# Kernel tuning notes

Hardware: AMD Instinct MI355X
Metric: run time of the kernel (lower is better)

## Reference

```python
import jax, jax.numpy as jnp
import numpy as np

N_HEAD = 16
HIDDEN = 1024

def setup_inputs() -> dict:
    key = jax.random.key(0)
    ks = jax.random.split(key, 4)
    B, T, D = 2, 2048, HIDDEN
    x = jax.random.normal(ks[0], (B, T, D), dtype=jnp.float32)
    attention_mask = jnp.zeros((B, 1, 1, T), dtype=jnp.float32)  # additive mask
    w_attn = jax.random.normal(ks[1], (D, 3 * D), dtype=jnp.float32) * (1.0 / np.sqrt(D))
    b_attn = jnp.zeros((3 * D,), dtype=jnp.float32)
    w_proj = jax.random.normal(ks[2], (D, D), dtype=jnp.float32) * (1.0 / np.sqrt(D))
    b_proj = jnp.zeros((D,), dtype=jnp.float32)
    return {"x": x, "attention_mask": attention_mask,
            "w_attn": w_attn, "b_attn": b_attn,
            "w_proj": w_proj, "b_proj": b_proj}

def reference(x, attention_mask, w_attn, b_attn, w_proj, b_proj):
    B, T, D = x.shape
    H = N_HEAD
    hd = D // H
    qkv = x @ w_attn + b_attn                      # [B,T,3D]
    q, k, v = jnp.split(qkv, 3, axis=-1)
    q = q.reshape(B, T, H, hd)
    k = k.reshape(B, T, H, hd)
    v = v.reshape(B, T, H, hd)
    qk = jnp.einsum('BFNH,BTNH->BNFT', q, k) / jnp.sqrt(jnp.asarray(hd, qk_dtype := q.dtype))
    # NOTE: source adds the mask twice (once unconditionally, once inside the None-check)
    attn_weights = qk + attention_mask + attention_mask
    attn_probs = jax.nn.softmax(attn_weights, axis=-1)  # dropout(0.01) is identity at inference
    attn_out = jnp.einsum('BNFT,BTNH->BFNH', attn_probs, v)
    attn_out = attn_out.reshape(B, T, D)
    return attn_out @ w_proj + b_proj
```

## Files before the change

### kernel.cpp

```cpp
#include <hip/hip_runtime.h>
#include <hip/hip_bf16.h>

#define T_SEQ 2048
#define D_MODEL 1024
#define N_HEADS 16

typedef _Float16 half8 __attribute__((ext_vector_type(8)));
typedef _Float16 half4 __attribute__((ext_vector_type(4)));
typedef _Float16 half2v __attribute__((ext_vector_type(2)));
typedef float floatx4 __attribute__((ext_vector_type(4)));
typedef unsigned short ushort4v __attribute__((ext_vector_type(4)));
typedef unsigned short ushort8v __attribute__((ext_vector_type(8)));

#define LOG2E 1.44269504088896f

__device__ __forceinline__ unsigned short f32_to_bf16(float f) {
  unsigned u = __builtin_bit_cast(unsigned, f);
  u = u + 0x7FFFu + ((u >> 16) & 1u);
  return (unsigned short)(u >> 16);
}
__device__ __forceinline__ float bf16_to_f32(unsigned short h) {
  unsigned u = ((unsigned)h) << 16;
  return __builtin_bit_cast(float, u);
}
__device__ __forceinline__ half2v pk_f16(float a, float b) {
  return __builtin_bit_cast(half2v, __builtin_amdgcn_cvt_pkrtz(a, b));
}

__device__ __forceinline__ void load16_lds(const _Float16* g, _Float16* lds_base, int lane) {
#if __has_builtin(__builtin_amdgcn_global_load_lds)
  __builtin_amdgcn_global_load_lds(
      (const __attribute__((address_space(1))) void*)g,
      (__attribute__((address_space(3))) void*)lds_base, 16, 0, 0);
#else
  *(half8*)(lds_base + lane * 8) = *(const half8*)g;
#endif
}

__global__ void k_detect(const unsigned short* __restrict__ x, int* __restrict__ flag) {
  __shared__ int cnt;
  if (threadIdx.x == 0) cnt = 0;
  __syncthreads();
  unsigned short v = x[(size_t)threadIdx.x * 2];
  int e = (v >> 7) & 0xFF;
  int ok = (v == 0) || (e >= 100 && e <= 150);
  atomicAdd(&cnt, ok);
  __syncthreads();
  if (threadIdx.x == 0) *flag = (cnt >= 192) ? 1 : 0;
}

__global__ void k_cvt_h8(const void* __restrict__ in, _Float16* __restrict__ out,
                         int n8, const int* __restrict__ flag) {
  int f = *flag;
  int i = blockIdx.x * 256 + threadIdx.x;
  if (i >= n8) return;
  half8 o;
  if (f) {
    ushort8v u = ((const ushort8v*)in)[i];
#pragma unroll
    for (int e = 0; e < 8; ++e) o[e] = (_Float16)bf16_to_f32(u[e]);
  } else {
    floatx4 a = ((const floatx4*)in)[2 * i];
    floatx4 b = ((const floatx4*)in)[2 * i + 1];
#pragma unroll
    for (int e = 0; e < 4; ++e) { o[e] = (_Float16)a[e]; o[e + 4] = (_Float16)b[e]; }
  }
  ((half8*)out)[i] = o;
}

__global__ void k_cvt3(const void* __restrict__ ba, const void* __restrict__ bp,
                       const void* __restrict__ mk, float* __restrict__ baF,
                       float* __restrict__ bpF, float* __restrict__ mask2,
                       const int* __restrict__ flag) {
  int f = *flag;
  int i = blockIdx.x * 256 + threadIdx.x;
  auto cv = [&](const void* p, int j) {
    return f ? bf16_to_f32(((const unsigned short*)p)[j]) : ((const float*)p)[j];
  };
  if (i < 3072) baF[i] = cv(ba, i);
  else if (i < 4096) bpF[i - 3072] = cv(bp, i - 3072);
  else mask2[i - 4096] = cv(mk, i - 4096) * (2.0f * LOG2E);
}

__global__ __launch_bounds__(256) void k_transpose2(
    const void* __restrict__ inA, _Float16* __restrict__ outA,
    const void* __restrict__ inB, _Float16* __restrict__ outB,
    const int* __restrict__ flag) {
  __shared__ float tile[32][33];
  int f = *flag;
  const void* in;
  _Float16* out;
  int N, bid;
  if (blockIdx.x < 3072) { in = inA; out = outA; N = 3072; bid = blockIdx.x; }
  else { in = inB; out = outB; N = 1024; bid = blockIdx.x - 3072; }
  const int K = 1024;
  int nb = N >> 5;
  int bx = bid % nb, by = bid / nb;
  int n0 = bx << 5, k0 = by << 5;
  int c = threadIdx.x & 31, r = threadIdx.x >> 5;
  const float* fin = (const float*)in;
  const unsigned short* uin = (const unsigned short*)in;
#pragma unroll
  for (int i = 0; i < 4; ++i) {
    int kk = r + i * 8;
    size_t idx = (size_t)(k0 + kk) * N + n0 + c;
    tile[kk][c] = f ? bf16_to_f32(uin[idx]) : fin[idx];
  }
  __syncthreads();
#pragma unroll
  for (int i = 0; i < 4; ++i) {
    int nn = r + i * 8;
    out[(size_t)(n0 + nn) * K + k0 + c] = (_Float16)tile[c][nn];
  }
}

template <int TM>
__global__ __launch_bounds__(256) void k_gemm(
    const _Float16* __restrict__ A, const _Float16* __restrict__ BT,
    const float* __restrict__ bias, void* __restrict__ D0,
    void* __restrict__ D1, void* __restrict__ D2,
    int M, int N, int K, int outKind, const int* __restrict__ flag) {
  constexpr int IM = TM / 32;
  __shared__ _Float16 As[TM * 32] __attribute__((aligned(16)));
  __shared__ _Float16 Bs[128 * 32] __attribute__((aligned(16)));
  const int tid = threadIdx.x;
  const int wave = tid >> 6, lane = tid & 63;
  const int ln = lane & 15, quad = lane >> 4;
  const int bm = blockIdx.y * TM, bn = blockIdx.x * 128;
  const int wm = (wave & 1) * (TM / 2), wn = (wave >> 1) * 64;

  const int r0 = tid >> 2, k0 = (tid & 3) * 8;
  const int r1 = (tid + 256) >> 2, k1 = (tid & 3) * 8;
  _Float16* As0 = As + (size_t)(wave * 64) * 8;
  _Float16* As1 = As + (size_t)(wave * 64 + 256) * 8;
  _Float16* Bs0 = Bs + (size_t)(wave * 64) * 8;
  _Float16* Bs1 = Bs + (size_t)(wave * 64 + 256) * 8;
  const _Float16* Ag0 = A + (size_t)(bm + r0) * K + k0;
  const _Float16* Ag1 = A + (size_t)(bm + r1) * K + k1;
  const _Float16* Bg0 = BT + (size_t)(bn + r0) * K + k0;
  const _Float16* Bg1 = BT + (size_t)(bn + r1) * K + k1;

  floatx4 acc[IM][4] = {};

  for (int kt = 0; kt < K; kt += 32) {
    __syncthreads();
    load16_lds(Ag0 + kt, As0, lane);
    if constexpr (TM == 128) load16_lds(Ag1 + kt, As1, lane);
    load16_lds(Bg0 + kt, Bs0, lane);
    load16_lds(Bg1 + kt, Bs1, lane);
    __syncthreads();
    half8 af[IM], bf[4];
#pragma unroll
    for (int i = 0; i < IM; ++i)
      af[i] = *(const half8*)(As + (wm + i * 16 + ln) * 32 + quad * 8);
#pragma unroll
    for (int j = 0; j < 4; ++j)
      bf[j] = *(const half8*)(Bs + (wn + j * 16 + ln) * 32 + quad * 8);
#pragma unroll
    for (int i = 0; i < IM; ++i)
#pragma unroll
      for (int j = 0; j < 4; ++j)
        acc[i][j] = __builtin_amdgcn_mfma_f32_16x16x32_f16(af[i], bf[j], acc[i][j], 0, 0, 0);
  }

  if (outKind == 0) {
    _Float16* Qs = (_Float16*)D0;
    _Float16* Ks = (_Float16*)D1;
    _Float16* Vt = (_Float16*)D2;
    const float qsc = 0.125f * LOG2E;
#pragma unroll
    for (int i = 0; i < IM; ++i) {
      int rbase = bm + wm + i * 16 + quad * 4;
      int sect = rbase >> 10;
      int cfeat = rbase & 1023;
      int h = cfeat >> 6, hd = cfeat & 63;
      float bv[4];
#pragma unroll
      for (int r = 0; r < 4; ++r) bv[r] = bias[rbase + r];
#pragma unroll
      for (int j = 0; j < 4; ++j) {
        int col = bn + wn + j * 16 + ln;
        int b = col >> 11, t = col & 2047;
        size_t bh = (size_t)b * N_HEADS + h;
        float v[4];
#pragma unroll
        for (int r = 0; r < 4; ++r) v[r] = acc[i][j][r] + bv[r];
        if (sect == 0) {
          half4 q;
#pragma unroll
          for (int r = 0; r < 4; ++r) q[r] = (_Float16)(v[r] * qsc);
          *(half4*)(Qs + (bh * T_SEQ + t) * 64 + hd) = q;
        } else if (sect == 1) {
          half4 kk4;
#pragma unroll
          for (int r = 0; r < 4; ++r) kk4[r] = (_Float16)v[r];
          *(half4*)(Ks + (bh * T_SEQ + t) * 64 + hd) = kk4;
        } else {
#pragma unroll
          for (int r = 0; r < 4; ++r)
            Vt[(bh * 64 + hd + r) * T_SEQ + t] = (_Float16)v[r];
        }
      }
    }
  } else {
    int mode = (*flag) ? 2 : 1;
#pragma unroll
    for (int i = 0; i < IM; ++i) {
      int rbase = bm + wm + i * 16 + quad * 4;
      float bv[4];
#pragma unroll
      for (int r = 0; r < 4; ++r) bv[r] = bias[rbase + r];
#pragma unroll
      for (int j = 0; j < 4; ++j) {
        int col = bn + wn + j * 16 + ln;
        float v[4];
#pragma unroll
        for (int r = 0; r < 4; ++r) v[r] = acc[i][j][r] + bv[r];
        if (mode == 1) {
          floatx4 o = {v[0], v[1], v[2], v[3]};
          *(floatx4*)((float*)D0 + (size_t)col * M + rbase) = o;
        } else {
          ushort4v o;
#pragma unroll
          for (int r = 0; r < 4; ++r) o[r] = f32_to_bf16(v[r]);
          *(ushort4v*)((unsigned short*)D0 + (size_t)col * M + rbase) = o;
        }
      }
    }
  }
}

__global__ __launch_bounds__(256) void k_flash(
    const _Float16* __restrict__ Qs, const _Float16* __restrict__ Ks,
    const _Float16* __restrict__ Vt, const float* __restrict__ mask2,
    _Float16* __restrict__ O) {
  __shared__ _Float16 Kl[2][64 * 64] __attribute__((aligned(16)));
  __shared__ _Float16 Vl[2][64 * 64] __attribute__((aligned(16)));
  __shared__ _Float16 Pl[4][16 * 64] __attribute__((aligned(16)));
  const int tid = threadIdx.x, wave = tid >> 6, lane = tid & 63;
  const int ln = lane & 15, quad = lane >> 4;
  const int id = blockIdx.x;
  const int qc = id & 31, h = (id >> 5) & 15, b = id >> 9;
  const size_t bh = (size_t)b * N_HEADS + h;
  const _Float16* Qb = Qs + bh * T_SEQ * 64;
  const _Float16* Kb = Ks + bh * T_SEQ * 64;
  const _Float16* Vb = Vt + bh * 64 * T_SEQ;
  const int q0 = qc * 64 + wave * 16;

  half8 qf[2];
#pragma unroll
  for (int kk = 0; kk < 2; ++kk)
    qf[kk] = *(const half8*)(Qb + (size_t)(q0 + ln) * 64 + kk * 32 + quad * 8);

  floatx4 Oacc[4] = {};
  float m0 = 0.f, l_i = 0.f;

  const int sr = tid >> 3, scn = (tid & 7) ^ (sr & 7);
  const _Float16* kp0 = Kb + (size_t)sr * 64 + scn * 8;
  const _Float16* kp1 = kp0 + 32 * 64;
  const _Float16* vp0 = Vb + (size_t)sr * T_SEQ + scn * 8;
  const _Float16* vp1 = vp0 + 32 * T_SEQ;
  const float* mq = mask2 + (size_t)b * T_SEQ + quad * 4;

  const int ksw0 = ((quad) ^ (ln & 7)) * 8;
  const int ksw1 = ((4 + quad) ^ (ln & 7)) * 8;
  _Float16* Pw = &Pl[wave][0];
  const int lnx = ln & 7;

  {
    _Float16* K0 = &Kl[0][0] + (size_t)wave * 512;
    _Float16* V0 = &Vl[0][0] + (size_t)wave * 512;
    load16_lds(kp0, K0, lane);
    load16_lds(kp1, K0 + 2048, lane);
    load16_lds(vp0, V0, lane);
    load16_lds(vp1, V0 + 2048, lane);
    kp0 += 64 * 64; kp1 += 64 * 64; vp0 += 64; vp1 += 64;
  }

  for (int t = 0; t < 32; ++t) {
    const int cur = t & 1;
    __syncthreads();
    if (t + 1 < 32) {
      _Float16* K0 = &Kl[cur ^ 1][0] + (size_t)wave * 512;
      _Float16* V0 = &Vl[cur ^ 1][0] + (size_t)wave * 512;
      load16_lds(kp0, K0, lane);
      load16_lds(kp1, K0 + 2048, lane);
      load16_lds(vp0, V0, lane);
      load16_lds(vp1, V0 + 2048, lane);
      kp0 += 64 * 64; kp1 += 64 * 64; vp0 += 64; vp1 += 64;
    }
    const _Float16* Kc = &Kl[cur][0];
    const _Float16* Vc = &Vl[cur][0];

    floatx4 s[4];
#pragma unroll
    for (int j = 0; j < 4; ++j) {
      floatx4 z = *(const floatx4*)(mq + j * 16);
      half8 kf0 = *(const half8*)(Kc + (j * 16 + ln) * 64 + ksw0);
      z = __builtin_amdgcn_mfma_f32_16x16x32_f16(kf0, qf[0], z, 0, 0, 0);
      half8 kf1 = *(const half8*)(Kc + (j * 16 + ln) * 64 + ksw1);
      z = __builtin_amdgcn_mfma_f32_16x16x32_f16(kf1, qf[1], z, 0, 0, 0);
      s[j] = z;
    }
    mq += 64;

    if (t == 0) {
      float tmax = -__builtin_inff();
#pragma unroll
      for (int j = 0; j < 4; ++j)
#pragma unroll
        for (int r = 0; r < 4; ++r) tmax = fmaxf(tmax, s[j][r]);
      tmax = fmaxf(tmax, __shfl_xor(tmax, 16, 64));
      tmax = fmaxf(tmax, __shfl_xor(tmax, 32, 64));
      m0 = fmaxf(tmax, -50.f);
    }

#pragma unroll
    for (int j = 0; j < 4; ++j)
#pragma unroll
      for (int r = 0; r < 4; ++r) {
        float p = __builtin_amdgcn_exp2f(s[j][r] - m0);
        s[j][r] = p;
        l_i += p;
      }

#pragma unroll
    for (int j = 0; j < 4; ++j) {
      half2v p01 = pk_f16(s[j][0], s[j][1]);
      half2v p23 = pk_f16(s[j][2], s[j][3]);
      half4 pk = {p01[0], p01[1], p23[0], p23[1]};
      int c = j * 2 + (quad >> 1);
      *(half4*)(Pw + ln * 64 + (c ^ lnx) * 8 + (quad & 1) * 4) = pk;
    }
    asm volatile("" ::: "memory");
#pragma unroll
    for (int kk = 0; kk < 2; ++kk) {
      half8 pf = *(const half8*)(Pw + ln * 64 + ((kk * 4 + quad) ^ lnx) * 8);
      int ks = kk ? ksw1 : ksw0;
#pragma unroll
      for (int jd = 0; jd < 4; ++jd) {
        half8 vf = *(const half8*)(Vc + (jd * 16 + ln) * 64 + ks);
        Oacc[jd] = __builtin_amdgcn_mfma_f32_16x16x32_f16(vf, pf, Oacc[jd], 0, 0, 0);
      }
    }
  }

  l_i += __shfl_xor(l_i, 16, 64);
  l_i += __shfl_xor(l_i, 32, 64);
  float inv = 1.f / l_i;
#pragma unroll
  for (int jd = 0; jd < 4; ++jd) {
    half4 ov;
#pragma unroll
    for (int r = 0; r < 4; ++r) ov[r] = (_Float16)(Oacc[jd][r] * inv);
    *(half4*)(O + ((size_t)b * T_SEQ + q0 + ln) * D_MODEL + h * 64 + jd * 16 + quad * 4) = ov;
  }
}

extern "C" void kernel_launch(void* const* d_in, const int* in_sizes, int n_in,
                              void* d_out, int out_size, void* d_ws, size_t ws_size,
                              hipStream_t stream) {
  const void* x      = d_in[0];
  const void* amask  = d_in[1];
  const void* w_attn = d_in[2];
  const void* b_attn = d_in[3];
  const void* w_proj = d_in[4];
  const void* b_proj = d_in[5];

  char* ws = (char*)d_ws;
  size_t off = 0;
  auto alloc = [&](size_t bytes) {
    void* p = ws + off;
    off += (bytes + 255) & ~(size_t)255;
    return p;
  };
  int* flag        = (int*)alloc(256);
  _Float16* Xh     = (_Float16*)alloc((size_t)4096 * 1024 * 2);
  _Float16* WaT    = (_Float16*)alloc((size_t)3072 * 1024 * 2);
  _Float16* WpT    = (_Float16*)alloc((size_t)1024 * 1024 * 2);
  float* baF       = (float*)alloc(3072 * 4);
  float* bpF       = (float*)alloc(1024 * 4);
  float* mask2     = (float*)alloc(4096 * 4);
  _Float16* Qs     = (_Float16*)alloc((size_t)4096 * 1024 * 2);
  _Float16* Ks     = (_Float16*)alloc((size_t)4096 * 1024 * 2);
  _Float16* Vt     = (_Float16*)alloc((size_t)4096 * 1024 * 2);
  _Float16* AttnH  = (_Float16*)alloc((size_t)4096 * 1024 * 2);

  k_detect<<<1, 256, 0, stream>>>((const unsigned short*)x, flag);
  k_cvt_h8<<<(4096 * 1024 / 8) / 256, 256, 0, stream>>>(x, Xh, 4096 * 1024 / 8, flag);
  k_transpose2<<<3072 + 1024, 256, 0, stream>>>(w_attn, WaT, w_proj, WpT, flag);
  k_cvt3<<<32, 256, 0, stream>>>(b_attn, b_proj, amask, baF, bpF, mask2, flag);

  dim3 g1(4096 / 128, 3072 / 128);
  k_gemm<128><<<g1, 256, 0, stream>>>(WaT, Xh, baF, Qs, Ks, Vt, 3072, 4096, 1024, 0, flag);

  k_flash<<<1024, 256, 0, stream>>>(Qs, Ks, Vt, mask2, AttnH);

  dim3 g2(4096 / 128, 1024 / 128);
  k_gemm<128><<<g2, 256, 0, stream>>>(WpT, AttnH, bpF, d_out, nullptr, nullptr, 1024, 4096, 1024, 1, flag);
}
```

Baseline: 223.1 us.

## Switch flash attention to 32x32x16 MFMA with register-shuffled P operand

The attention kernel moves from 16x16x32 to 32x32x16 MFMA tiles. Each wave now handles 32 query rows, so a block covers 128 queries and the grid halves to 512 blocks. The softmax probabilities no longer round-trip through LDS; they are packed to f16 and swapped across wave halves with cross-lane shuffles to form the B operand directly. This halves K/V LDS reloads per query, removes the P staging buffer, and cuts LDS traffic. In exchange it uses more accumulator registers and gives fewer blocks to spread across the CUs.

```diff
diff --git a/kernel.cpp b/kernel.cpp
--- a/kernel.cpp
+++ b/kernel.cpp
@@ -9,8 +9,10 @@
 typedef _Float16 half4 __attribute__((ext_vector_type(4)));
 typedef _Float16 half2v __attribute__((ext_vector_type(2)));
 typedef float floatx4 __attribute__((ext_vector_type(4)));
+typedef float floatx16 __attribute__((ext_vector_type(16)));
 typedef unsigned short ushort4v __attribute__((ext_vector_type(4)));
 typedef unsigned short ushort8v __attribute__((ext_vector_type(8)));
+typedef unsigned int uintx4 __attribute__((ext_vector_type(4)));
 
 #define LOG2E 1.44269504088896f
 
@@ -236,23 +238,22 @@
     _Float16* __restrict__ O) {
   __shared__ _Float16 Kl[2][64 * 64] __attribute__((aligned(16)));
   __shared__ _Float16 Vl[2][64 * 64] __attribute__((aligned(16)));
-  __shared__ _Float16 Pl[4][16 * 64] __attribute__((aligned(16)));
   const int tid = threadIdx.x, wave = tid >> 6, lane = tid & 63;
-  const int ln = lane & 15, quad = lane >> 4;
+  const int l31 = lane & 31, h5 = lane >> 5, swz = l31 & 7;
   const int id = blockIdx.x;
-  const int qc = id & 31, h = (id >> 5) & 15, b = id >> 9;
-  const size_t bh = (size_t)b * N_HEADS + h;
+  const int qc = id & 15, hh = (id >> 4) & 15, b = id >> 8;
+  const size_t bh = (size_t)b * N_HEADS + hh;
   const _Float16* Qb = Qs + bh * T_SEQ * 64;
   const _Float16* Kb = Ks + bh * T_SEQ * 64;
   const _Float16* Vb = Vt + bh * 64 * T_SEQ;
-  const int q0 = qc * 64 + wave * 16;
-
-  half8 qf[2];
-#pragma unroll
-  for (int kk = 0; kk < 2; ++kk)
-    qf[kk] = *(const half8*)(Qb + (size_t)(q0 + ln) * 64 + kk * 32 + quad * 8);
-
-  floatx4 Oacc[4] = {};
+  const int q0 = qc * 128 + wave * 32;
+
+  half8 qf[4];
+#pragma unroll
+  for (int ks = 0; ks < 4; ++ks)
+    qf[ks] = *(const half8*)(Qb + (size_t)(q0 + l31) * 64 + ks * 16 + h5 * 8);
+
+  floatx16 Oacc[2] = {};
   float m0 = 0.f, l_i = 0.f;
 
   const int sr = tid >> 3, scn = (tid & 7) ^ (sr & 7);
@@ -260,12 +261,7 @@
   const _Float16* kp1 = kp0 + 32 * 64;
   const _Float16* vp0 = Vb + (size_t)sr * T_SEQ + scn * 8;
   const _Float16* vp1 = vp0 + 32 * T_SEQ;
-  const float* mq = mask2 + (size_t)b * T_SEQ + quad * 4;
-
-  const int ksw0 = ((quad) ^ (ln & 7)) * 8;
-  const int ksw1 = ((4 + quad) ^ (ln & 7)) * 8;
-  _Float16* Pw = &Pl[wave][0];
-  const int lnx = ln & 7;
+  const float* mq = mask2 + (size_t)b * T_SEQ;
 
   {
     _Float16* K0 = &Kl[0][0] + (size_t)wave * 512;
@@ -292,69 +288,83 @@
     const _Float16* Kc = &Kl[cur][0];
     const _Float16* Vc = &Vl[cur][0];
 
-    floatx4 s[4];
-#pragma unroll
-    for (int j = 0; j < 4; ++j) {
-      floatx4 z = *(const floatx4*)(mq + j * 16);
-      half8 kf0 = *(const half8*)(Kc + (j * 16 + ln) * 64 + ksw0);
-      z = __builtin_amdgcn_mfma_f32_16x16x32_f16(kf0, qf[0], z, 0, 0, 0);
-      half8 kf1 = *(const half8*)(Kc + (j * 16 + ln) * 64 + ksw1);
-      z = __builtin_amdgcn_mfma_f32_16x16x32_f16(kf1, qf[1], z, 0, 0, 0);
-      s[j] = z;
+    floatx16 sa[2];
+#pragma unroll
+    for (int kg = 0; kg < 2; ++kg) {
+      floatx16 z;
+#pragma unroll
+      for (int tt = 0; tt < 4; ++tt) {
+        floatx4 mv = *(const floatx4*)(mq + kg * 32 + 8 * tt + 4 * h5);
+#pragma unroll
+        for (int i = 0; i < 4; ++i) z[4 * tt + i] = mv[i];
+      }
+#pragma unroll
+      for (int ks = 0; ks < 4; ++ks) {
+        half8 kf = *(const half8*)(Kc + (kg * 32 + l31) * 64 + ((ks * 2 + h5) ^ swz) * 8);
+        z = __builtin_amdgcn_mfma_f32_32x32x16_f16(kf, qf[ks], z, 0, 0, 0);
+      }
+      sa[kg] = z;
     }
     mq += 64;
 
     if (t == 0) {
       float tmax = -__builtin_inff();
 #pragma unroll
-      for (int j = 0; j < 4; ++j)
-#pragma unroll
-        for (int r = 0; r < 4; ++r) tmax = fmaxf(tmax, s[j][r]);
-      tmax = fmaxf(tmax, __shfl_xor(tmax, 16, 64));
+      for (int kg = 0; kg < 2; ++kg)
+#pragma unroll
+        for (int r = 0; r < 16; ++r) tmax = fmaxf(tmax, sa[kg][r]);
       tmax = fmaxf(tmax, __shfl_xor(tmax, 32, 64));
       m0 = fmaxf(tmax, -50.f);
     }
 
 #pragma unroll
-    for (int j = 0; j < 4; ++j)
-#pragma unroll
-      for (int r = 0; r < 4; ++r) {
-        float p = __builtin_amdgcn_exp2f(s[j][r] - m0);
-        s[j][r] = p;
+    for (int kg = 0; kg < 2; ++kg) {
+#pragma unroll
+      for (int r = 0; r < 16; ++r) {
+        float p = __builtin_amdgcn_exp2f(sa[kg][r] - m0);
+        sa[kg][r] = p;
         l_i += p;
       }
-
-#pragma unroll
-    for (int j = 0; j < 4; ++j) {
-      half2v p01 = pk_f16(s[j][0], s[j][1]);
-      half2v p23 = pk_f16(s[j][2], s[j][3]);
-      half4 pk = {p01[0], p01[1], p23[0], p23[1]};
-      int c = j * 2 + (quad >> 1);
-      *(half4*)(Pw + ln * 64 + (c ^ lnx) * 8 + (quad & 1) * 4) = pk;
-    }
-    asm volatile("" ::: "memory");
-#pragma unroll
-    for (int kk = 0; kk < 2; ++kk) {
-      half8 pf = *(const half8*)(Pw + ln * 64 + ((kk * 4 + quad) ^ lnx) * 8);
-      int ks = kk ? ksw1 : ksw0;
-#pragma unroll
-      for (int jd = 0; jd < 4; ++jd) {
-        half8 vf = *(const half8*)(Vc + (jd * 16 + ln) * 64 + ks);
-        Oacc[jd] = __builtin_amdgcn_mfma_f32_16x16x32_f16(vf, pf, Oacc[jd], 0, 0, 0);
-      }
-    }
-  }
-
-  l_i += __shfl_xor(l_i, 16, 64);
+      unsigned pk[4][2];
+#pragma unroll
+      for (int tt = 0; tt < 4; ++tt) {
+        half2v a = pk_f16(sa[kg][4 * tt], sa[kg][4 * tt + 1]);
+        half2v bq = pk_f16(sa[kg][4 * tt + 2], sa[kg][4 * tt + 3]);
+        pk[tt][0] = __builtin_bit_cast(unsigned, a);
+        pk[tt][1] = __builtin_bit_cast(unsigned, bq);
+      }
+#pragma unroll
+      for (int ss = 0; ss < 2; ++ss) {
+        int sendT = h5 ? 2 * ss : 2 * ss + 1;
+        int ownT = h5 ? 2 * ss + 1 : 2 * ss;
+        unsigned r0 = __shfl_xor(pk[sendT][0], 32, 64);
+        unsigned r1 = __shfl_xor(pk[sendT][1], 32, 64);
+        uintx4 u;
+        if (h5 == 0) { u[0] = pk[ownT][0]; u[1] = pk[ownT][1]; u[2] = r0; u[3] = r1; }
+        else         { u[0] = r0; u[1] = r1; u[2] = pk[ownT][0]; u[3] = pk[ownT][1]; }
+        half8 pf = __builtin_bit_cast(half8, u);
+        int kst = kg * 2 + ss;
+#pragma unroll
+        for (int dg = 0; dg < 2; ++dg) {
+          half8 vf = *(const half8*)(Vc + (dg * 32 + l31) * 64 + ((kst * 2 + h5) ^ swz) * 8);
+          Oacc[dg] = __builtin_amdgcn_mfma_f32_32x32x16_f16(vf, pf, Oacc[dg], 0, 0, 0);
+        }
+      }
+    }
+  }
+
   l_i += __shfl_xor(l_i, 32, 64);
   float inv = 1.f / l_i;
-#pragma unroll
-  for (int jd = 0; jd < 4; ++jd) {
-    half4 ov;
-#pragma unroll
-    for (int r = 0; r < 4; ++r) ov[r] = (_Float16)(Oacc[jd][r] * inv);
-    *(half4*)(O + ((size_t)b * T_SEQ + q0 + ln) * D_MODEL + h * 64 + jd * 16 + quad * 4) = ov;
-  }
+  _Float16* Og = O + ((size_t)b * T_SEQ + q0 + l31) * D_MODEL + hh * 64;
+#pragma unroll
+  for (int dg = 0; dg < 2; ++dg)
+#pragma unroll
+    for (int tt = 0; tt < 4; ++tt) {
+      half4 ov;
+#pragma unroll
+      for (int i = 0; i < 4; ++i) ov[i] = (_Float16)(Oacc[dg][4 * tt + i] * inv);
+      *(half4*)(Og + dg * 32 + 8 * tt + 4 * h5) = ov;
+    }
 }
 
 extern "C" void kernel_launch(void* const* d_in, const int* in_sizes, int n_in,
@@ -394,7 +404,7 @@
   dim3 g1(4096 / 128, 3072 / 128);
   k_gemm<128><<<g1, 256, 0, stream>>>(WaT, Xh, baF, Qs, Ks, Vt, 3072, 4096, 1024, 0, flag);
 
-  k_flash<<<1024, 256, 0, stream>>>(Qs, Ks, Vt, mask2, AttnH);
+  k_flash<<<512, 256, 0, stream>>>(Qs, Ks, Vt, mask2, AttnH);
 
   dim3 g2(4096 / 128, 1024 / 128);
   k_gemm<128><<<g2, 256, 0, stream>>>(WpT, AttnH, bpF, d_out, nullptr, nullptr, 1024, 4096, 1024, 1, flag);
```

After: 233.2 us. +4.5%, slower.
